# Performance work log

Hardware: AMD Instinct MI355X
Metric: run time of the kernel (lower is better)

Reference implementation:

```python
import jax, jax.numpy as jnp
import numpy as np

EPS = 1e-15

def setup_inputs() -> dict:
    key = jax.random.key(0)
    k1, k2, k3 = jax.random.split(key, 3)
    B, N, F, C = 8, 2048, 256, 64
    x = jax.random.normal(k1, (B, N, F), dtype=jnp.float32)
    adj = jax.random.uniform(k2, (B, N, N), dtype=jnp.float32)
    mask = jnp.ones((B, N), dtype=bool)
    W = jax.random.normal(k3, (F, C), dtype=jnp.float32) * 0.05
    b = jnp.zeros((C,), dtype=jnp.float32)
    return {"x": x, "adj": adj, "mask": mask, "W": W, "b": b}


def reference(x, adj, mask, W, b):
    B, N, F = x.shape
    C = W.shape[1]
    # MLP (single linear, no act/norm), dropout=0 (eval), softmax
    s = jax.nn.softmax(x @ W + b, axis=-1)                 # [B,N,C]
    m_f = mask.astype(x.dtype)[..., None]                  # [B,N,1]
    x = x * m_f
    s = s * m_f
    st = jnp.swapaxes(s, 1, 2)                             # [B,C,N]
    out = jax.nn.selu(st @ x)                              # [B,C,F]
    out_adj = st @ adj @ s                                 # [B,C,C]
    degrees = jnp.sum(adj, axis=-1)[..., None] * m_f       # [B,N,1]
    m = jnp.sum(degrees, axis=(1, 2)) / 2                  # [B]
    ca = st @ degrees                                      # [B,C,1]
    cb = jnp.swapaxes(degrees, 1, 2) @ s                   # [B,1,C]
    normalizer = (ca @ cb) / 2 / m[:, None, None]          # [B,C,C]
    decompose = out_adj - normalizer
    spectral_loss = jnp.mean(-jnp.trace(decompose, axis1=-2, axis2=-1) / 2 / m)
    ss = st @ s                                            # [B,C,C]
    i_s = jnp.eye(C, dtype=ss.dtype)
    ss_n = jnp.linalg.norm(ss, axis=(-2, -1), keepdims=True)
    i_n = jnp.linalg.norm(i_s)                             # sqrt(C)
    ortho_loss = jnp.mean(jnp.linalg.norm(ss / ss_n - i_s / i_n, axis=(-2, -1)))
    cluster_size = jnp.sum(s, axis=1)                      # [B,C]
    # note: torch broadcasts [B] / [B,1] -> [B,B]; reproduce faithfully
    cl = jnp.linalg.norm(cluster_size, axis=1) / jnp.sum(m_f, axis=1) * i_n - 1
    cluster_loss = jnp.mean(cl)
    ind = jnp.arange(C)
    out_adj = out_adj.at[:, ind, ind].set(0.0)
    d = jnp.sqrt(jnp.sum(out_adj, axis=-1))[:, None] + EPS  # [B,1,C]
    out_adj = out_adj / d / jnp.swapaxes(d, 1, 2)
    return (s, out, out_adj, spectral_loss, ortho_loss, cluster_loss)
```

## Files before the change

### kernel.cpp

```cpp
#include <hip/hip_runtime.h>
#include <math.h>

#define NB 8
#define NN 2048
#define NF 256
#define NC 64

typedef short bf16x8 __attribute__((ext_vector_type(8)));
typedef float f32x4  __attribute__((ext_vector_type(4)));

#define OFF_S    0
#define OFF_OUT  (NB*NN*NC)
#define OFF_OADJ (OFF_OUT + NB*NC*NF)
#define OFF_SCAL (OFF_OADJ + NB*NC*NC)

#define WS_T    0
#define WS_DEG  (2*NB*NN*NC)
#define WS_SF   (WS_DEG + 4*NB*NN)
#define WS_POUT (WS_SF + NB*32*8*64*4)
#define WS_PADJ (WS_POUT + NB*4*16*4096)
#define WS_PSS  (WS_PADJ + NB*32*4096)
#define WS_PCS  (WS_PSS  + NB*32*4096)
#define WS_RADJ (WS_PCS  + NB*32*64)
#define WS_RSS  (WS_RADJ + NB*4096)
#define WS_RCS  (WS_RSS  + NB*4096)
#define WS_BS   (WS_RCS  + NB*64)

__device__ __forceinline__ unsigned short f2bf(float f) {
    union { float f; unsigned int u; } v; v.f = f;
    unsigned int u = v.u;
    return (unsigned short)((u + 0x7FFFu + ((u >> 16) & 1u)) >> 16);
}
__device__ __forceinline__ float bf2f(unsigned short h) {
    union { unsigned int u; float f; } v; v.u = ((unsigned int)h) << 16;
    return v.f;
}

__global__ __launch_bounds__(512) void k_fused_s(
    const float* __restrict__ x, const float* __restrict__ W,
    const float* __restrict__ bias, float* __restrict__ s_out,
    unsigned short* __restrict__ sfrag, float* __restrict__ P_ss,
    float* __restrict__ P_cs)
{
    const int ch = blockIdx.x & 31;
    const int b  = blockIdx.x >> 5;
    const int n0 = ch * 64;
    __shared__ float xs[64][260];
    __shared__ float sB[64][68];
    __shared__ float csP[8][68];
    const int t = threadIdx.x, w = t >> 6, l = t & 63;
    const float* X = x + ((size_t)b * NN + n0) * NF;

    #pragma unroll
    for (int r = 0; r < 8; ++r) {
        const int row = w * 8 + r;
        *(float4*)&xs[row][l * 4] = *(const float4*)&X[(size_t)row * NF + l * 4];
    }
    const float bz = bias[l];
    float acc[8];
    #pragma unroll
    for (int r = 0; r < 8; ++r) acc[r] = bz;
    #pragma unroll 4
    for (int k4 = 0; k4 < 64; ++k4) {
        const int k = k4 * 4;
        const float w0 = W[(k + 0) * NC + l], w1 = W[(k + 1) * NC + l],
                    w2 = W[(k + 2) * NC + l], w3 = W[(k + 3) * NC + l];
        #pragma unroll
        for (int r = 0; r < 8; ++r) {
            const float4 xv = *(const float4*)&xs[w * 8 + r][k];
            acc[r] = fmaf(xv.x, w0, acc[r]); acc[r] = fmaf(xv.y, w1, acc[r]);
            acc[r] = fmaf(xv.z, w2, acc[r]); acc[r] = fmaf(xv.w, w3, acc[r]);
        }
    }
    float cs_acc = 0.f;
    #pragma unroll
    for (int r = 0; r < 8; ++r) {
        float a = acc[r], mx = a;
        #pragma unroll
        for (int off = 32; off; off >>= 1) mx = fmaxf(mx, __shfl_xor(mx, off));
        const float e = __expf(a - mx);
        float sum = e;
        #pragma unroll
        for (int off = 32; off; off >>= 1) sum += __shfl_xor(sum, off);
        const float sv = e / sum;
        s_out[((size_t)b * NN + n0 + w * 8 + r) * NC + l] = sv;
        sB[w * 8 + r][l] = sv;
        cs_acc += sv;
    }
    csP[w][l] = cs_acc;
    __syncthreads();

    {
        const int n = w >> 1, kk = w & 1;
        const int col = 16 * n + (l & 15);
        const int kb  = 32 * kk + (l >> 4) * 8;
        unsigned short tmp[8];
        #pragma unroll
        for (int r = 0; r < 8; ++r) tmp[r] = f2bf(sB[kb + r][col]);
        *(uint4*)&sfrag[((((size_t)(b * 32 + ch)) * 8 + w) * 64 + l) * 8] = *(uint4*)tmp;
    }
    {
        const int c0 = (t >> 5) * 4;
        const int c2 = (t & 31) * 2;
        float a2[4][2] = {{0.f,0.f},{0.f,0.f},{0.f,0.f},{0.f,0.f}};
        #pragma unroll 8
        for (int n = 0; n < 64; ++n) {
            const float4 av = *(const float4*)&sB[n][c0];
            const float2 bv = *(const float2*)&sB[n][c2];
            const float av_[4] = {av.x, av.y, av.z, av.w};
            #pragma unroll
            for (int i = 0; i < 4; ++i) {
                a2[i][0] = fmaf(av_[i], bv.x, a2[i][0]);
                a2[i][1] = fmaf(av_[i], bv.y, a2[i][1]);
            }
        }
        float* Ps = P_ss + (size_t)(b * 32 + ch) * 4096;
        #pragma unroll
        for (int i = 0; i < 4; ++i) {
            float2 v; v.x = a2[i][0]; v.y = a2[i][1];
            *(float2*)&Ps[(c0 + i) * 64 + c2] = v;
        }
    }
    if (t < 64) {
        float v = 0.f;
        #pragma unroll
        for (int g = 0; g < 8; ++g) v += csP[g][t];
        P_cs[(b * 32 + ch) * 64 + t] = v;
    }
}

__global__ __launch_bounds__(256, 4) void k_adj_reg(
    const float* __restrict__ adj, const unsigned short* __restrict__ sfrag,
    unsigned short* __restrict__ Tbuf4, float* __restrict__ deg4)
{
    const int h  = blockIdx.x & 3;
    const int mt = (blockIdx.x >> 2) & 31;
    const int b  = blockIdx.x >> 7;
    const int m0 = mt * 64;
    const int t = threadIdx.x, w = t >> 6, l = t & 63;
    const int row = m0 + 16 * w + (l & 15);
    const float* Arow = adj + (size_t)b * NN * NN + (size_t)row * NN + h * 512 + (l >> 4) * 8;
    const unsigned short* BF = sfrag + ((size_t)(b * 32 + h * 8)) * 8 * 64 * 8 + (size_t)l * 8;

    f32x4 acc[4] = {};
    float dsum = 0.f;
    float4 a0 = *(const float4*)&Arow[0];
    float4 a1 = *(const float4*)&Arow[4];
    #pragma unroll 2
    for (int ks = 0; ks < 16; ++ks) {
        float4 p0v = a0, p1v = a1;
        if (ks < 15) {
            p0v = *(const float4*)&Arow[(ks + 1) * 32];
            p1v = *(const float4*)&Arow[(ks + 1) * 32 + 4];
        }
        dsum += a0.x + a0.y + a0.z + a0.w + a1.x + a1.y + a1.z + a1.w;
        unsigned q0, q1, q2, q3;
        asm("v_cvt_pk_bf16_f32 %0, %1, %2" : "=v"(q0) : "v"(a0.x), "v"(a0.y));
        asm("v_cvt_pk_bf16_f32 %0, %1, %2" : "=v"(q1) : "v"(a0.z), "v"(a0.w));
        asm("v_cvt_pk_bf16_f32 %0, %1, %2" : "=v"(q2) : "v"(a1.x), "v"(a1.y));
        asm("v_cvt_pk_bf16_f32 %0, %1, %2" : "=v"(q3) : "v"(a1.z), "v"(a1.w));
        uint4 af_u; af_u.x = q0; af_u.y = q1; af_u.z = q2; af_u.w = q3;
        const bf16x8 af = *(const bf16x8*)&af_u;
        const unsigned short* Bk = BF + ((size_t)((ks >> 1) * 8 + (ks & 1))) * 64 * 8;
        #pragma unroll
        for (int n = 0; n < 4; ++n) {
            const bf16x8 bfv = *(const bf16x8*)&Bk[(size_t)(n * 2) * 64 * 8];
            acc[n] = __builtin_amdgcn_mfma_f32_16x16x32_bf16(af, bfv, acc[n], 0, 0, 0);
        }
        a0 = p0v; a1 = p1v;
    }
    unsigned short* Tw = Tbuf4 + (((size_t)b * NN + m0 + 16 * w) * 4 + h) * 64;
    #pragma unroll
    for (int n = 0; n < 4; ++n)
        #pragma unroll
        for (int j = 0; j < 4; ++j)
            Tw[(size_t)((l >> 4) * 4 + j) * 256 + n * 16 + (l & 15)] = f2bf(acc[n][j]);
    dsum += __shfl_xor(dsum, 16);
    dsum += __shfl_xor(dsum, 32);
    if (l < 16)
        deg4[(size_t)(h * NB + b) * NN + m0 + 16 * w + l] = dsum;
}

__global__ __launch_bounds__(256) void k_stx(
    const float* __restrict__ x, const float* __restrict__ s,
    float* __restrict__ P_out)
{
    const int ch = blockIdx.x & 15;
    const int ft = (blockIdx.x >> 4) & 3;
    const int b  = blockIdx.x >> 6;

    __shared__ float sL[64][68];
    __shared__ float xL[64][68];

    const int t  = threadIdx.x;
    const int lr = t >> 6;
    const int lc = t & 63;
    const int tr = t >> 4;
    const int tc = t & 15;
    const int r0 = tr * 4, c0 = tc * 4;

    const float* S = s + (size_t)b * NN * NC;
    const float* X = x + (size_t)b * NN * NF + ft * 64;

    float acc[4][4] = {{0.f,0.f,0.f,0.f},{0.f,0.f,0.f,0.f},{0.f,0.f,0.f,0.f},{0.f,0.f,0.f,0.f}};

    for (int tile = 0; tile < 2; ++tile) {
        const int nb = ch * 128 + tile * 64;
        __syncthreads();
        #pragma unroll
        for (int k = 0; k < 16; ++k) {
            const int nn = lr + 4 * k;
            sL[nn][lc] = S[(size_t)(nb + nn) * NC + lc];
            xL[nn][lc] = X[(size_t)(nb + nn) * NF + lc];
        }
        __syncthreads();
        #pragma unroll 8
        for (int n = 0; n < 64; ++n) {
            const float4 av = *(const float4*)&sL[n][r0];
            const float4 bv = *(const float4*)&xL[n][c0];
            const float av_[4] = {av.x, av.y, av.z, av.w};
            const float bv_[4] = {bv.x, bv.y, bv.z, bv.w};
            #pragma unroll
            for (int i = 0; i < 4; ++i)
                #pragma unroll
                for (int j = 0; j < 4; ++j)
                    acc[i][j] = fmaf(av_[i], bv_[j], acc[i][j]);
        }
    }
    float* P = P_out + (size_t)blockIdx.x * 4096;
    #pragma unroll
    for (int i = 0; i < 4; ++i) {
        float4 v; v.x = acc[i][0]; v.y = acc[i][1]; v.z = acc[i][2]; v.w = acc[i][3];
        *(float4*)&P[(r0 + i) * 64 + c0] = v;
    }
}

__global__ __launch_bounds__(256) void k_red_cc(
    const float* __restrict__ s, const unsigned short* __restrict__ Tbuf4,
    float* __restrict__ P_adj)
{
    const int ch = blockIdx.x & 31;
    const int b  = blockIdx.x >> 5;
    const int nb = ch * 64;

    __shared__ float sL[64][68];
    __shared__ float tL[64][68];

    const int t  = threadIdx.x;
    const int lr = t >> 6;
    const int lc = t & 63;
    const int tr = t >> 4;
    const int tc = t & 15;
    const int r0 = tr * 4, c0 = tc * 4;

    const float* S = s + (size_t)b * NN * NC;

    float aadj[4][4] = {{0.f,0.f,0.f,0.f},{0.f,0.f,0.f,0.f},{0.f,0.f,0.f,0.f},{0.f,0.f,0.f,0.f}};

    #pragma unroll
    for (int k = 0; k < 16; ++k) {
        const int nn = lr + 4 * k;
        sL[nn][lc] = S[(size_t)(nb + nn) * NC + lc];
        const unsigned short* Tp = &Tbuf4[(((size_t)b * NN + nb + nn) * 4) * 64 + lc];
        tL[nn][lc] = bf2f(Tp[0]) + bf2f(Tp[64]) + bf2f(Tp[128]) + bf2f(Tp[192]);
    }
    __syncthreads();
    #pragma unroll 8
    for (int n = 0; n < 64; ++n) {
        const float4 av = *(const float4*)&sL[n][r0];
        const float4 tv = *(const float4*)&tL[n][c0];
        const float av_[4] = {av.x, av.y, av.z, av.w};
        const float tv_[4] = {tv.x, tv.y, tv.z, tv.w};
        #pragma unroll
        for (int i = 0; i < 4; ++i)
            #pragma unroll
            for (int j = 0; j < 4; ++j)
                aadj[i][j] = fmaf(av_[i], tv_[j], aadj[i][j]);
    }
    float* Pa = P_adj + (size_t)(b * 32 + ch) * 4096;
    #pragma unroll
    for (int i = 0; i < 4; ++i) {
        float4 v; v.x = aadj[i][0]; v.y = aadj[i][1]; v.z = aadj[i][2]; v.w = aadj[i][3];
        *(float4*)&Pa[(r0 + i) * 64 + c0] = v;
    }
}

__global__ __launch_bounds__(256) void k_reduce2(
    const float* __restrict__ Pout, const float* __restrict__ P_adj,
    const float* __restrict__ P_ss, const float* __restrict__ P_cs,
    float* __restrict__ out, float* __restrict__ Radj, float* __restrict__ Rss,
    float* __restrict__ Rcs)
{
    const int bid = blockIdx.x;
    const int t = threadIdx.x;
    if (bid < 512) {
        const int idx = bid * 256 + t;
        const int f  = idx & 255;
        const int cc = (idx >> 8) & 63;
        const int b  = idx >> 14;
        const int ft = f >> 6, ff = f & 63;
        const float* P = Pout + ((size_t)(b * 4 + ft) * 16) * 4096 + cc * 64 + ff;
        float v = 0.f;
        #pragma unroll
        for (int ch = 0; ch < 16; ++ch) v += P[(size_t)ch * 4096];
        const float scale = 1.0507009873554805f, alpha = 1.6732632423543772f;
        out[idx] = (v > 0.f) ? scale * v : scale * alpha * expm1f(v);
    } else if (bid < 768) {
        const int idx = (bid - 512) * 256 + t;
        const int arr = idx >> 15;
        const int rem = idx & 32767;
        const int b   = rem >> 12;
        const int e   = rem & 4095;
        const float* P = (arr == 0 ? P_adj : P_ss) + (size_t)(b * 32) * 4096 + e;
        float v = 0.f;
        #pragma unroll
        for (int ch = 0; ch < 32; ++ch) v += P[(size_t)ch * 4096];
        (arr == 0 ? Radj : Rss)[b * 4096 + e] = v;
    } else {
        for (int e = t; e < 512; e += 256) {
            const int b = e >> 6, c = e & 63;
            const float* P = P_cs + (size_t)(b * 32) * 64 + c;
            float v = 0.f;
            #pragma unroll
            for (int ch = 0; ch < 32; ++ch) v += P[ch * 64];
            Rcs[b * 64 + c] = v;
        }
    }
}

__device__ __forceinline__ float block_sum(float v, float* red)
{
    #pragma unroll
    for (int off = 32; off; off >>= 1) v += __shfl_xor(v, off);
    const int w = threadIdx.x >> 6;
    __syncthreads();
    if ((threadIdx.x & 63) == 0) red[w] = v;
    __syncthreads();
    return red[0] + red[1] + red[2] + red[3];
}

__global__ __launch_bounds__(256) void k_finalize(
    const float* __restrict__ Radj, const float* __restrict__ Rss,
    const float* __restrict__ Rcs, const float* __restrict__ deg4,
    const float* __restrict__ s,
    float* __restrict__ oadj_out, float* __restrict__ bscal)
{
    const int b = blockIdx.x;
    const int t = threadIdx.x;
    __shared__ float oadj[64][65];
    __shared__ float ssm [64][65];
    __shared__ float degL[NN];
    __shared__ float caP[16][68];
    __shared__ float ca[64], cs[64], dd[64];
    __shared__ float red[4];

    for (int e = t; e < 4096; e += 256) {
        const int i = e >> 6, j = e & 63;
        oadj[i][j] = Radj[(size_t)b * 4096 + e];
        ssm [i][j] = Rss [(size_t)b * 4096 + e];
    }
    if (t < 64) cs[t] = Rcs[b * 64 + t];

    float dsum = 0.f;
    for (int n = t; n < NN; n += 256) {
        float dv = 0.f;
        #pragma unroll
        for (int p = 0; p < 4; ++p)
            dv += deg4[(size_t)(p * NB + b) * NN + n];
        degL[n] = dv;
        dsum += dv;
    }
    const float m = 0.5f * block_sum(dsum, red);

    {
        const int c4 = (t & 15) * 4;
        const int g  = t >> 4;
        const float* S = s + (size_t)b * NN * NC;
        float cacc[4] = {0.f, 0.f, 0.f, 0.f};
        for (int i = 0; i < 128; ++i) {
            const int n = g * 128 + i;
            const float4 sv = *(const float4*)&S[(size_t)n * NC + c4];
            const float dv = degL[n];
            cacc[0] = fmaf(sv.x, dv, cacc[0]);
            cacc[1] = fmaf(sv.y, dv, cacc[1]);
            cacc[2] = fmaf(sv.z, dv, cacc[2]);
            cacc[3] = fmaf(sv.w, dv, cacc[3]);
        }
        #pragma unroll
        for (int j = 0; j < 4; ++j) caP[g][c4 + j] = cacc[j];
        __syncthreads();
        if (t < 64) {
            float v = 0.f;
            #pragma unroll
            for (int g2 = 0; g2 < 16; ++g2) v += caP[g2][t];
            ca[t] = v;
        }
    }

    float tv = (t < 64) ? oadj[t][t] : 0.f;
    const float tr_oadj = block_sum(tv, red);
    float cv = (t < 64) ? ca[t] * ca[t] : 0.f;
    const float ca2 = block_sum(cv, red);

    float ss2p = 0.f;
    for (int e = t; e < 4096; e += 256) {
        const float q = ssm[e >> 6][e & 63];
        ss2p += q * q;
    }
    const float ssn = sqrtf(block_sum(ss2p, red));
    float op = 0.f;
    for (int e = t; e < 4096; e += 256) {
        const int i = e >> 6, j = e & 63;
        const float d0 = ssm[i][j] / ssn - ((i == j) ? 0.125f : 0.f);
        op += d0 * d0;
    }
    const float ortho_b = sqrtf(block_sum(op, red));
    float c2 = (t < 64) ? cs[t] * cs[t] : 0.f;
    const float cnorm_b = sqrtf(block_sum(c2, red));

    if (t == 0) {
        const float trn = ca2 / (2.f * m);
        bscal[b]          = -(tr_oadj - trn) / (2.f * m);
        bscal[NB + b]     = ortho_b;
        bscal[2 * NB + b] = cnorm_b;
    }

    __syncthreads();
    if (t < 64) oadj[t][t] = 0.f;
    __syncthreads();
    if (t < 64) {
        float rs = 0.f;
        #pragma unroll 8
        for (int j = 0; j < 64; ++j) rs += oadj[t][j];
        dd[t] = sqrtf(rs) + 1e-15f;
    }
    __syncthreads();
    float* O = oadj_out + (size_t)b * 4096;
    for (int e = t; e < 4096; e += 256) {
        const int i = e >> 6, j = e & 63;
        O[e] = oadj[i][j] / (dd[i] * dd[j]);
    }
}

__global__ void k_scalars(const float* __restrict__ bscal, float* __restrict__ scal_out)
{
    if (threadIdx.x == 0 && blockIdx.x == 0) {
        float sp = 0.f, orth = 0.f, cn = 0.f;
        for (int b = 0; b < NB; ++b) {
            sp   += bscal[b];
            orth += bscal[NB + b];
            cn   += bscal[2 * NB + b];
        }
        scal_out[0] = sp / NB;
        scal_out[1] = orth / NB;
        scal_out[2] = (cn / NB) * 8.0f / 2048.0f - 1.0f;
    }
}

extern "C" void kernel_launch(void* const* d_in, const int* in_sizes, int n_in,
                              void* d_out, int out_size, void* d_ws, size_t ws_size,
                              hipStream_t stream)
{
    const float* x    = (const float*)d_in[0];
    const float* adj  = (const float*)d_in[1];
    const float* W    = (const float*)d_in[3];
    const float* bias = (const float*)d_in[4];

    float* out = (float*)d_out;
    float* ws  = (float*)d_ws;

    float*          s_out = out + OFF_S;
    unsigned short* Tbuf4 = (unsigned short*)(ws + WS_T);
    float*          deg4  = ws + WS_DEG;
    unsigned short* sfrag = (unsigned short*)(ws + WS_SF);
    float*          Pout  = ws + WS_POUT;
    float*          Padj  = ws + WS_PADJ;
    float*          Pss   = ws + WS_PSS;
    float*          Pcs   = ws + WS_PCS;
    float*          Radj  = ws + WS_RADJ;
    float*          Rss   = ws + WS_RSS;
    float*          Rcs   = ws + WS_RCS;
    float*          bscal = ws + WS_BS;

    k_fused_s <<<NB * 32,     512, 0, stream>>>(x, W, bias, s_out, sfrag, Pss, Pcs);
    k_adj_reg <<<NB * 32 * 4, 256, 0, stream>>>(adj, sfrag, Tbuf4, deg4);
    k_stx     <<<NB * 4 * 16, 256, 0, stream>>>(x, s_out, Pout);
    k_red_cc  <<<NB * 32,     256, 0, stream>>>(s_out, Tbuf4, Padj);
    k_reduce2 <<<769,         256, 0, stream>>>(Pout, Padj, Pss, Pcs,
                                                out + OFF_OUT, Radj, Rss, Rcs);
    k_finalize<<<NB,          256, 0, stream>>>(Radj, Rss, Rcs, deg4, s_out,
                                                out + OFF_OADJ, bscal);
    k_scalars <<<1, 64, 0, stream>>>(bscal, out + OFF_SCAL);
}
```

Measured before the change: 89.81 us.

## Use split-bf16 MFMA for logits, merge adj/stx and reduction kernels

Computes x@W with MFMA using a hi/lo bf16 split of x and a pre-packed W, in place of scalar FP32 FMAs. The S^T S partial is also done with MFMA. The adjacency GEMM and the S^T x GEMM are merged into one launch, with deeper prefetch on the adj loads. The ca term (S^T deg) moves out of the single-block-per-batch finalize into the parallel reduction stage, and the reduce kernels are regrouped. This adds a small W-packing kernel and gives up some precision in the logits and the ss terms.

Result: faster. 85.90 us (-4.3%).

```diff
diff --git a/kernel.cpp b/kernel.cpp
--- a/kernel.cpp
+++ b/kernel.cpp
@@ -17,13 +17,16 @@
 #define WS_T    0
 #define WS_DEG  (2*NB*NN*NC)
 #define WS_SF   (WS_DEG + 4*NB*NN)
-#define WS_POUT (WS_SF + NB*32*8*64*4)
+#define WS_WF   (WS_SF + NB*32*8*64*4)
+#define WS_POUT (WS_WF + 16384)
 #define WS_PADJ (WS_POUT + NB*4*16*4096)
 #define WS_PSS  (WS_PADJ + NB*32*4096)
-#define WS_PCS  (WS_PSS  + NB*32*4096)
+#define WS_PCA  (WS_PSS  + NB*32*4096)
+#define WS_PCS  (WS_PCA  + NB*32*64)
 #define WS_RADJ (WS_PCS  + NB*32*64)
 #define WS_RSS  (WS_RADJ + NB*4096)
-#define WS_RCS  (WS_RSS  + NB*4096)
+#define WS_RCA  (WS_RSS  + NB*4096)
+#define WS_RCS  (WS_RCA  + NB*64)
 #define WS_BS   (WS_RCS  + NB*64)
 
 __device__ __forceinline__ unsigned short f2bf(float f) {
@@ -36,265 +39,330 @@
     return v.f;
 }
 
-__global__ __launch_bounds__(512) void k_fused_s(
-    const float* __restrict__ x, const float* __restrict__ W,
-    const float* __restrict__ bias, float* __restrict__ s_out,
-    unsigned short* __restrict__ sfrag, float* __restrict__ P_ss,
-    float* __restrict__ P_cs)
+__global__ __launch_bounds__(256) void k_wpack(
+    const float* __restrict__ W, unsigned short* __restrict__ Wfh,
+    unsigned short* __restrict__ Wfl)
+{
+    const int ks = blockIdx.x;
+    const int t = threadIdx.x;
+    const int n = t >> 6, l = t & 63;
+    const int col = 16 * n + (l & 15), g = l >> 4;
+    unsigned short th[8], tl[8];
+    #pragma unroll
+    for (int r = 0; r < 8; ++r) {
+        const int j = ((r >> 2) << 4) + g * 4 + (r & 3);
+        const float wv = W[(32 * ks + j) * NC + col];
+        const unsigned short h = f2bf(wv);
+        th[r] = h;
+        tl[r] = f2bf(wv - bf2f(h));
+    }
+    const size_t off = (((size_t)ks * 4 + n) * 64 + l) * 8;
+    *(uint4*)&Wfh[off] = *(uint4*)th;
+    *(uint4*)&Wfl[off] = *(uint4*)tl;
+}
+
+__global__ __launch_bounds__(256) void k_fused_s(
+    const float* __restrict__ x, const unsigned short* __restrict__ Wfh,
+    const unsigned short* __restrict__ Wfl, const float* __restrict__ bias,
+    float* __restrict__ s_out, unsigned short* __restrict__ sfrag,
+    float* __restrict__ P_ss, float* __restrict__ P_cs)
 {
     const int ch = blockIdx.x & 31;
     const int b  = blockIdx.x >> 5;
     const int n0 = ch * 64;
-    __shared__ float xs[64][260];
+    __shared__ __align__(16) unsigned short xh[64 * 256];
+    __shared__ __align__(16) unsigned short xl[64 * 256];
     __shared__ float sB[64][68];
-    __shared__ float csP[8][68];
+    __shared__ __align__(16) unsigned short sfl[8 * 64 * 8];
+    __shared__ float csP[16][64];
     const int t = threadIdx.x, w = t >> 6, l = t & 63;
-    const float* X = x + ((size_t)b * NN + n0) * NF;
+
+    {
+        const int srow = t >> 2, sq = t & 3;
+        const float* Xr = x + ((size_t)(b * NN + n0 + srow)) * NF;
+        float4 xv[16];
+        #pragma unroll
+        for (int i = 0; i < 16; ++i) xv[i] = *(const float4*)&Xr[i * 16 + sq * 4];
+        #pragma unroll
+        for (int i = 0; i < 16; ++i) {
+            const float4 v = xv[i];
+            const unsigned short h0 = f2bf(v.x), h1 = f2bf(v.y),
+                                 h2 = f2bf(v.z), h3 = f2bf(v.w);
+            const unsigned short e0 = f2bf(v.x - bf2f(h0)), e1 = f2bf(v.y - bf2f(h1)),
+                                 e2 = f2bf(v.z - bf2f(h2)), e3 = f2bf(v.w - bf2f(h3));
+            const int e = srow * 256 + (i >> 1) * 32 + sq * 8 + (i & 1) * 4;
+            const int byt = (2 * e) ^ ((srow & 7) << 4);
+            uint2 hv; hv.x = h0 | ((unsigned)h1 << 16); hv.y = h2 | ((unsigned)h3 << 16);
+            uint2 lv; lv.x = e0 | ((unsigned)e1 << 16); lv.y = e2 | ((unsigned)e3 << 16);
+            *(uint2*)((char*)xh + byt) = hv;
+            *(uint2*)((char*)xl + byt) = lv;
+        }
+    }
+    __syncthreads();
+
+    f32x4 acc[4] = {};
+    {
+        const int row = 16 * w + (l & 15);
+        const int g16 = (l >> 4) * 16;
+        #pragma unroll
+        for (int ks = 0; ks < 8; ++ks) {
+            const int addr = (row * 512 + ks * 64 + g16) ^ ((row & 7) << 4);
+            const bf16x8 ah = *(const bf16x8*)((const char*)xh + addr);
+            const bf16x8 al = *(const bf16x8*)((const char*)xl + addr);
+            #pragma unroll
+            for (int n = 0; n < 4; ++n) {
+                const size_t off = (((size_t)ks * 4 + n) * 64 + l) * 8;
+                const bf16x8 bh = *(const bf16x8*)&Wfh[off];
+                const bf16x8 bl = *(const bf16x8*)&Wfl[off];
+                acc[n] = __builtin_amdgcn_mfma_f32_16x16x32_bf16(ah, bh, acc[n], 0, 0, 0);
+                acc[n] = __builtin_amdgcn_mfma_f32_16x16x32_bf16(ah, bl, acc[n], 0, 0, 0);
+                acc[n] = __builtin_amdgcn_mfma_f32_16x16x32_bf16(al, bh, acc[n], 0, 0, 0);
+            }
+        }
+    }
+
+    {
+        float bz[4];
+        #pragma unroll
+        for (int n = 0; n < 4; ++n) bz[n] = bias[16 * n + (l & 15)];
+        const int g = l >> 4;
+        float ex[4][4], sj[4];
+        #pragma unroll
+        for (int j = 0; j < 4; ++j) {
+            float m = acc[0][j] + bz[0];
+            #pragma unroll
+            for (int n = 1; n < 4; ++n) m = fmaxf(m, acc[n][j] + bz[n]);
+            #pragma unroll
+            for (int k = 1; k < 16; k <<= 1) m = fmaxf(m, __shfl_xor(m, k));
+            float s = 0.f;
+            #pragma unroll
+            for (int n = 0; n < 4; ++n) { ex[n][j] = __expf(acc[n][j] + bz[n] - m); s += ex[n][j]; }
+            #pragma unroll
+            for (int k = 1; k < 16; k <<= 1) s += __shfl_xor(s, k);
+            sj[j] = 1.f / s;
+        }
+        #pragma unroll
+        for (int n = 0; n < 4; ++n) {
+            float csn = 0.f;
+            #pragma unroll
+            for (int j = 0; j < 4; ++j) {
+                const float sv = ex[n][j] * sj[j];
+                sB[16 * w + g * 4 + j][16 * n + (l & 15)] = sv;
+                csn += sv;
+            }
+            csP[w * 4 + g][16 * n + (l & 15)] = csn;
+        }
+    }
+    __syncthreads();
 
     #pragma unroll
-    for (int r = 0; r < 8; ++r) {
-        const int row = w * 8 + r;
-        *(float4*)&xs[row][l * 4] = *(const float4*)&X[(size_t)row * NF + l * 4];
-    }
-    const float bz = bias[l];
-    float acc[8];
-    #pragma unroll
-    for (int r = 0; r < 8; ++r) acc[r] = bz;
-    #pragma unroll 4
-    for (int k4 = 0; k4 < 64; ++k4) {
-        const int k = k4 * 4;
-        const float w0 = W[(k + 0) * NC + l], w1 = W[(k + 1) * NC + l],
-                    w2 = W[(k + 2) * NC + l], w3 = W[(k + 3) * NC + l];
+    for (int p = 0; p < 2; ++p) {
+        const int c2 = w + p * 4;
+        const int n = c2 >> 1, kk = c2 & 1;
+        const int col = 16 * n + (l & 15), g = l >> 4;
+        unsigned short tmp[8];
         #pragma unroll
         for (int r = 0; r < 8; ++r) {
-            const float4 xv = *(const float4*)&xs[w * 8 + r][k];
-            acc[r] = fmaf(xv.x, w0, acc[r]); acc[r] = fmaf(xv.y, w1, acc[r]);
-            acc[r] = fmaf(xv.z, w2, acc[r]); acc[r] = fmaf(xv.w, w3, acc[r]);
-        }
-    }
-    float cs_acc = 0.f;
-    #pragma unroll
-    for (int r = 0; r < 8; ++r) {
-        float a = acc[r], mx = a;
-        #pragma unroll
-        for (int off = 32; off; off >>= 1) mx = fmaxf(mx, __shfl_xor(mx, off));
-        const float e = __expf(a - mx);
-        float sum = e;
-        #pragma unroll
-        for (int off = 32; off; off >>= 1) sum += __shfl_xor(sum, off);
-        const float sv = e / sum;
-        s_out[((size_t)b * NN + n0 + w * 8 + r) * NC + l] = sv;
-        sB[w * 8 + r][l] = sv;
-        cs_acc += sv;
-    }
-    csP[w][l] = cs_acc;
-    __syncthreads();
-
+            const int j = ((r >> 2) << 4) + g * 4 + (r & 3);
+            tmp[r] = f2bf(sB[32 * kk + j][col]);
+        }
+        const size_t fo = ((size_t)c2 * 64 + l) * 8;
+        *(uint4*)&sfl[fo] = *(uint4*)tmp;
+        *(uint4*)&sfrag[((size_t)(b * 32 + ch)) * 8 * 64 * 8 + fo] = *(uint4*)tmp;
+    }
     {
-        const int n = w >> 1, kk = w & 1;
-        const int col = 16 * n + (l & 15);
-        const int kb  = 32 * kk + (l >> 4) * 8;
-        unsigned short tmp[8];
-        #pragma unroll
-        for (int r = 0; r < 8; ++r) tmp[r] = f2bf(sB[kb + r][col]);
-        *(uint4*)&sfrag[((((size_t)(b * 32 + ch)) * 8 + w) * 64 + l) * 8] = *(uint4*)tmp;
-    }
+        const int row = t >> 2, q = t & 3;
+        float4 o[4];
+        #pragma unroll
+        for (int ii = 0; ii < 4; ++ii) o[ii] = *(const float4*)&sB[row][q * 16 + ii * 4];
+        float* So = s_out + ((size_t)(b * NN + n0 + row)) * NC + q * 16;
+        #pragma unroll
+        for (int ii = 0; ii < 4; ++ii) *(float4*)&So[ii * 4] = o[ii];
+    }
+    __syncthreads();
+
     {
-        const int c0 = (t >> 5) * 4;
-        const int c2 = (t & 31) * 2;
-        float a2[4][2] = {{0.f,0.f},{0.f,0.f},{0.f,0.f},{0.f,0.f}};
-        #pragma unroll 8
-        for (int n = 0; n < 64; ++n) {
-            const float4 av = *(const float4*)&sB[n][c0];
-            const float2 bv = *(const float2*)&sB[n][c2];
-            const float av_[4] = {av.x, av.y, av.z, av.w};
-            #pragma unroll
-            for (int i = 0; i < 4; ++i) {
-                a2[i][0] = fmaf(av_[i], bv.x, a2[i][0]);
-                a2[i][1] = fmaf(av_[i], bv.y, a2[i][1]);
-            }
+        f32x4 a2[4] = {};
+        const bf16x8 af0 = *(const bf16x8*)&sfl[((size_t)(w * 2 + 0) * 64 + l) * 8];
+        const bf16x8 af1 = *(const bf16x8*)&sfl[((size_t)(w * 2 + 1) * 64 + l) * 8];
+        #pragma unroll
+        for (int n = 0; n < 4; ++n) {
+            const bf16x8 b0 = *(const bf16x8*)&sfl[((size_t)(n * 2 + 0) * 64 + l) * 8];
+            const bf16x8 b1 = *(const bf16x8*)&sfl[((size_t)(n * 2 + 1) * 64 + l) * 8];
+            a2[n] = __builtin_amdgcn_mfma_f32_16x16x32_bf16(af0, b0, a2[n], 0, 0, 0);
+            a2[n] = __builtin_amdgcn_mfma_f32_16x16x32_bf16(af1, b1, a2[n], 0, 0, 0);
         }
         float* Ps = P_ss + (size_t)(b * 32 + ch) * 4096;
         #pragma unroll
-        for (int i = 0; i < 4; ++i) {
-            float2 v; v.x = a2[i][0]; v.y = a2[i][1];
-            *(float2*)&Ps[(c0 + i) * 64 + c2] = v;
-        }
+        for (int n = 0; n < 4; ++n)
+            #pragma unroll
+            for (int j = 0; j < 4; ++j)
+                Ps[(16 * w + (l >> 4) * 4 + j) * 64 + 16 * n + (l & 15)] = a2[n][j];
     }
     if (t < 64) {
         float v = 0.f;
         #pragma unroll
-        for (int g = 0; g < 8; ++g) v += csP[g][t];
+        for (int g2 = 0; g2 < 16; ++g2) v += csP[g2][t];
         P_cs[(b * 32 + ch) * 64 + t] = v;
     }
 }
 
-__global__ __launch_bounds__(256, 4) void k_adj_reg(
+__global__ __launch_bounds__(256, 4) void k_adjstx(
     const float* __restrict__ adj, const unsigned short* __restrict__ sfrag,
-    unsigned short* __restrict__ Tbuf4, float* __restrict__ deg4)
-{
-    const int h  = blockIdx.x & 3;
-    const int mt = (blockIdx.x >> 2) & 31;
-    const int b  = blockIdx.x >> 7;
-    const int m0 = mt * 64;
-    const int t = threadIdx.x, w = t >> 6, l = t & 63;
-    const int row = m0 + 16 * w + (l & 15);
-    const float* Arow = adj + (size_t)b * NN * NN + (size_t)row * NN + h * 512 + (l >> 4) * 8;
-    const unsigned short* BF = sfrag + ((size_t)(b * 32 + h * 8)) * 8 * 64 * 8 + (size_t)l * 8;
-
-    f32x4 acc[4] = {};
-    float dsum = 0.f;
-    float4 a0 = *(const float4*)&Arow[0];
-    float4 a1 = *(const float4*)&Arow[4];
-    #pragma unroll 2
-    for (int ks = 0; ks < 16; ++ks) {
-        float4 p0v = a0, p1v = a1;
-        if (ks < 15) {
-            p0v = *(const float4*)&Arow[(ks + 1) * 32];
-            p1v = *(const float4*)&Arow[(ks + 1) * 32 + 4];
-        }
-        dsum += a0.x + a0.y + a0.z + a0.w + a1.x + a1.y + a1.z + a1.w;
-        unsigned q0, q1, q2, q3;
-        asm("v_cvt_pk_bf16_f32 %0, %1, %2" : "=v"(q0) : "v"(a0.x), "v"(a0.y));
-        asm("v_cvt_pk_bf16_f32 %0, %1, %2" : "=v"(q1) : "v"(a0.z), "v"(a0.w));
-        asm("v_cvt_pk_bf16_f32 %0, %1, %2" : "=v"(q2) : "v"(a1.x), "v"(a1.y));
-        asm("v_cvt_pk_bf16_f32 %0, %1, %2" : "=v"(q3) : "v"(a1.z), "v"(a1.w));
-        uint4 af_u; af_u.x = q0; af_u.y = q1; af_u.z = q2; af_u.w = q3;
-        const bf16x8 af = *(const bf16x8*)&af_u;
-        const unsigned short* Bk = BF + ((size_t)((ks >> 1) * 8 + (ks & 1))) * 64 * 8;
-        #pragma unroll
-        for (int n = 0; n < 4; ++n) {
-            const bf16x8 bfv = *(const bf16x8*)&Bk[(size_t)(n * 2) * 64 * 8];
-            acc[n] = __builtin_amdgcn_mfma_f32_16x16x32_bf16(af, bfv, acc[n], 0, 0, 0);
-        }
-        a0 = p0v; a1 = p1v;
-    }
-    unsigned short* Tw = Tbuf4 + (((size_t)b * NN + m0 + 16 * w) * 4 + h) * 64;
-    #pragma unroll
-    for (int n = 0; n < 4; ++n)
-        #pragma unroll
-        for (int j = 0; j < 4; ++j)
-            Tw[(size_t)((l >> 4) * 4 + j) * 256 + n * 16 + (l & 15)] = f2bf(acc[n][j]);
-    dsum += __shfl_xor(dsum, 16);
-    dsum += __shfl_xor(dsum, 32);
-    if (l < 16)
-        deg4[(size_t)(h * NB + b) * NN + m0 + 16 * w + l] = dsum;
-}
-
-__global__ __launch_bounds__(256) void k_stx(
     const float* __restrict__ x, const float* __restrict__ s,
+    unsigned short* __restrict__ Tbuf4, float* __restrict__ deg4,
     float* __restrict__ P_out)
 {
-    const int ch = blockIdx.x & 15;
-    const int ft = (blockIdx.x >> 4) & 3;
-    const int b  = blockIdx.x >> 6;
-
-    __shared__ float sL[64][68];
-    __shared__ float xL[64][68];
-
-    const int t  = threadIdx.x;
-    const int lr = t >> 6;
-    const int lc = t & 63;
-    const int tr = t >> 4;
-    const int tc = t & 15;
-    const int r0 = tr * 4, c0 = tc * 4;
-
-    const float* S = s + (size_t)b * NN * NC;
-    const float* X = x + (size_t)b * NN * NF + ft * 64;
-
-    float acc[4][4] = {{0.f,0.f,0.f,0.f},{0.f,0.f,0.f,0.f},{0.f,0.f,0.f,0.f},{0.f,0.f,0.f,0.f}};
-
-    for (int tile = 0; tile < 2; ++tile) {
-        const int nb = ch * 128 + tile * 64;
-        __syncthreads();
+    const int bid = blockIdx.x;
+    const int t = threadIdx.x;
+    if (bid < 1024) {
+        const int h = bid & 3, mt = (bid >> 2) & 31, b = bid >> 7;
+        const int m0 = mt * 64;
+        const int w = t >> 6, l = t & 63, g = l >> 4;
+        const int row = m0 + 16 * w + (l & 15);
+        const float* A = adj + (size_t)b * NN * NN + (size_t)row * NN + h * 512 + g * 4;
+        const unsigned short* BF = sfrag + ((size_t)(b * 32 + h * 8)) * 8 * 64 * 8 + (size_t)l * 8;
+
+        f32x4 acc[4] = {};
+        float dsum = 0.f;
+        float4 c0a = *(const float4*)&A[0],  c0b = *(const float4*)&A[16];
+        float4 c1a = *(const float4*)&A[32], c1b = *(const float4*)&A[48];
+        for (int ks = 0; ks < 16; ++ks) {
+            float4 n2a = c0a, n2b = c0b;
+            if (ks < 14) {
+                n2a = *(const float4*)&A[(ks + 2) * 32];
+                n2b = *(const float4*)&A[(ks + 2) * 32 + 16];
+            }
+            dsum += c0a.x + c0a.y + c0a.z + c0a.w + c0b.x + c0b.y + c0b.z + c0b.w;
+            unsigned q0, q1, q2, q3;
+            asm("v_cvt_pk_bf16_f32 %0, %1, %2" : "=v"(q0) : "v"(c0a.x), "v"(c0a.y));
+            asm("v_cvt_pk_bf16_f32 %0, %1, %2" : "=v"(q1) : "v"(c0a.z), "v"(c0a.w));
+            asm("v_cvt_pk_bf16_f32 %0, %1, %2" : "=v"(q2) : "v"(c0b.x), "v"(c0b.y));
+            asm("v_cvt_pk_bf16_f32 %0, %1, %2" : "=v"(q3) : "v"(c0b.z), "v"(c0b.w));
+            uint4 afu; afu.x = q0; afu.y = q1; afu.z = q2; afu.w = q3;
+            const bf16x8 af = *(const bf16x8*)&afu;
+            const unsigned short* Bk = BF + ((size_t)((ks >> 1) * 8 + (ks & 1))) * 64 * 8;
+            #pragma unroll
+            for (int n = 0; n < 4; ++n) {
+                const bf16x8 bfv = *(const bf16x8*)&Bk[(size_t)(n * 2) * 64 * 8];
+                acc[n] = __builtin_amdgcn_mfma_f32_16x16x32_bf16(af, bfv, acc[n], 0, 0, 0);
+            }
+            c0a = c1a; c0b = c1b; c1a = n2a; c1b = n2b;
+        }
+        unsigned short* Tw = Tbuf4 + (((size_t)b * NN + m0 + 16 * w) * 4 + h) * 64;
+        #pragma unroll
+        for (int n = 0; n < 4; ++n)
+            #pragma unroll
+            for (int j = 0; j < 4; ++j)
+                Tw[(size_t)((l >> 4) * 4 + j) * 256 + n * 16 + (l & 15)] = f2bf(acc[n][j]);
+        dsum += __shfl_xor(dsum, 16);
+        dsum += __shfl_xor(dsum, 32);
+        if (l < 16)
+            deg4[(size_t)(h * NB + b) * NN + m0 + 16 * w + l] = dsum;
+    } else {
+        const int sb = bid - 1024;
+        const int ch = sb & 15, ft = (sb >> 4) & 3, b = sb >> 6;
+        __shared__ float sL[64][68];
+        __shared__ float xL[64][68];
+        const int lr = t >> 6, lc = t & 63;
+        const int r0 = (t >> 4) * 4, c0 = (t & 15) * 4;
+        const float* S = s + (size_t)b * NN * NC;
+        const float* X = x + (size_t)b * NN * NF + ft * 64;
+        float acc[4][4] = {{0,0,0,0},{0,0,0,0},{0,0,0,0},{0,0,0,0}};
+        for (int tile = 0; tile < 2; ++tile) {
+            const int nb = ch * 128 + tile * 64;
+            __syncthreads();
+            #pragma unroll
+            for (int k = 0; k < 16; ++k) {
+                const int nn = lr + 4 * k;
+                sL[nn][lc] = S[(size_t)(nb + nn) * NC + lc];
+                xL[nn][lc] = X[(size_t)(nb + nn) * NF + lc];
+            }
+            __syncthreads();
+            #pragma unroll 8
+            for (int n = 0; n < 64; ++n) {
+                const float4 av = *(const float4*)&sL[n][r0];
+                const float4 bv = *(const float4*)&xL[n][c0];
+                const float av_[4] = {av.x, av.y, av.z, av.w};
+                const float bv_[4] = {bv.x, bv.y, bv.z, bv.w};
+                #pragma unroll
+                for (int i = 0; i < 4; ++i)
+                    #pragma unroll
+                    for (int j = 0; j < 4; ++j)
+                        acc[i][j] = fmaf(av_[i], bv_[j], acc[i][j]);
+            }
+        }
+        float* P = P_out + (size_t)sb * 4096;
+        #pragma unroll
+        for (int i = 0; i < 4; ++i) {
+            float4 v; v.x = acc[i][0]; v.y = acc[i][1]; v.z = acc[i][2]; v.w = acc[i][3];
+            *(float4*)&P[(r0 + i) * 64 + c0] = v;
+        }
+    }
+}
+
+__global__ __launch_bounds__(256) void k_redmix(
+    const float* __restrict__ s, const unsigned short* __restrict__ Tbuf4,
+    const float* __restrict__ deg4, const float* __restrict__ Pout,
+    float* __restrict__ P_adj, float* __restrict__ P_ca, float* __restrict__ out)
+{
+    const int bid = blockIdx.x;
+    const int t = threadIdx.x;
+    if (bid < 256) {
+        const int ch = bid & 31, b = bid >> 5;
+        const int nb = ch * 64;
+        __shared__ float sL[64][68];
+        __shared__ float tL[64][68];
+        __shared__ float dL[64];
+        const int lr = t >> 6, lc = t & 63;
+        const int tr = t >> 4, tc = t & 15;
+        const int r0 = tr * 4, c0 = tc * 4;
+        const float* S = s + (size_t)b * NN * NC;
+        float aadj[4][4] = {{0,0,0,0},{0,0,0,0},{0,0,0,0},{0,0,0,0}};
+        float aca[4] = {0.f, 0.f, 0.f, 0.f};
         #pragma unroll
         for (int k = 0; k < 16; ++k) {
             const int nn = lr + 4 * k;
             sL[nn][lc] = S[(size_t)(nb + nn) * NC + lc];
-            xL[nn][lc] = X[(size_t)(nb + nn) * NF + lc];
+            const unsigned short* Tp = &Tbuf4[(((size_t)b * NN + nb + nn) * 4) * 64 + lc];
+            tL[nn][lc] = bf2f(Tp[0]) + bf2f(Tp[64]) + bf2f(Tp[128]) + bf2f(Tp[192]);
+        }
+        if (t < 64) {
+            float dv = 0.f;
+            #pragma unroll
+            for (int p = 0; p < 4; ++p)
+                dv += deg4[(size_t)(p * NB + b) * NN + nb + t];
+            dL[t] = dv;
         }
         __syncthreads();
-        #pragma unroll 8
+        #pragma unroll 4
         for (int n = 0; n < 64; ++n) {
             const float4 av = *(const float4*)&sL[n][r0];
-            const float4 bv = *(const float4*)&xL[n][c0];
+            const float4 tv = *(const float4*)&tL[n][c0];
+            const float dv  = dL[n];
             const float av_[4] = {av.x, av.y, av.z, av.w};
-            const float bv_[4] = {bv.x, bv.y, bv.z, bv.w};
-            #pragma unroll
-            for (int i = 0; i < 4; ++i)
+            const float tv_[4] = {tv.x, tv.y, tv.z, tv.w};
+            #pragma unroll
+            for (int i = 0; i < 4; ++i) {
+                aca[i] = fmaf(av_[i], dv, aca[i]);
                 #pragma unroll
                 for (int j = 0; j < 4; ++j)
-                    acc[i][j] = fmaf(av_[i], bv_[j], acc[i][j]);
-        }
-    }
-    float* P = P_out + (size_t)blockIdx.x * 4096;
-    #pragma unroll
-    for (int i = 0; i < 4; ++i) {
-        float4 v; v.x = acc[i][0]; v.y = acc[i][1]; v.z = acc[i][2]; v.w = acc[i][3];
-        *(float4*)&P[(r0 + i) * 64 + c0] = v;
-    }
-}
-
-__global__ __launch_bounds__(256) void k_red_cc(
-    const float* __restrict__ s, const unsigned short* __restrict__ Tbuf4,
-    float* __restrict__ P_adj)
-{
-    const int ch = blockIdx.x & 31;
-    const int b  = blockIdx.x >> 5;
-    const int nb = ch * 64;
-
-    __shared__ float sL[64][68];
-    __shared__ float tL[64][68];
-
-    const int t  = threadIdx.x;
-    const int lr = t >> 6;
-    const int lc = t & 63;
-    const int tr = t >> 4;
-    const int tc = t & 15;
-    const int r0 = tr * 4, c0 = tc * 4;
-
-    const float* S = s + (size_t)b * NN * NC;
-
-    float aadj[4][4] = {{0.f,0.f,0.f,0.f},{0.f,0.f,0.f,0.f},{0.f,0.f,0.f,0.f},{0.f,0.f,0.f,0.f}};
-
-    #pragma unroll
-    for (int k = 0; k < 16; ++k) {
-        const int nn = lr + 4 * k;
-        sL[nn][lc] = S[(size_t)(nb + nn) * NC + lc];
-        const unsigned short* Tp = &Tbuf4[(((size_t)b * NN + nb + nn) * 4) * 64 + lc];
-        tL[nn][lc] = bf2f(Tp[0]) + bf2f(Tp[64]) + bf2f(Tp[128]) + bf2f(Tp[192]);
-    }
-    __syncthreads();
-    #pragma unroll 8
-    for (int n = 0; n < 64; ++n) {
-        const float4 av = *(const float4*)&sL[n][r0];
-        const float4 tv = *(const float4*)&tL[n][c0];
-        const float av_[4] = {av.x, av.y, av.z, av.w};
-        const float tv_[4] = {tv.x, tv.y, tv.z, tv.w};
-        #pragma unroll
-        for (int i = 0; i < 4; ++i)
-            #pragma unroll
-            for (int j = 0; j < 4; ++j)
-                aadj[i][j] = fmaf(av_[i], tv_[j], aadj[i][j]);
-    }
-    float* Pa = P_adj + (size_t)(b * 32 + ch) * 4096;
-    #pragma unroll
-    for (int i = 0; i < 4; ++i) {
-        float4 v; v.x = aadj[i][0]; v.y = aadj[i][1]; v.z = aadj[i][2]; v.w = aadj[i][3];
-        *(float4*)&Pa[(r0 + i) * 64 + c0] = v;
-    }
-}
-
-__global__ __launch_bounds__(256) void k_reduce2(
-    const float* __restrict__ Pout, const float* __restrict__ P_adj,
-    const float* __restrict__ P_ss, const float* __restrict__ P_cs,
-    float* __restrict__ out, float* __restrict__ Radj, float* __restrict__ Rss,
-    float* __restrict__ Rcs)
-{
-    const int bid = blockIdx.x;
-    const int t = threadIdx.x;
-    if (bid < 512) {
-        const int idx = bid * 256 + t;
+                    aadj[i][j] = fmaf(av_[i], tv_[j], aadj[i][j]);
+            }
+        }
+        float* Pa = P_adj + (size_t)(b * 32 + ch) * 4096;
+        #pragma unroll
+        for (int i = 0; i < 4; ++i) {
+            float4 v; v.x = aadj[i][0]; v.y = aadj[i][1]; v.z = aadj[i][2]; v.w = aadj[i][3];
+            *(float4*)&Pa[(r0 + i) * 64 + c0] = v;
+        }
+        if (tc == 0) {
+            #pragma unroll
+            for (int i = 0; i < 4; ++i)
+                P_ca[(b * 32 + ch) * 64 + r0 + i] = aca[i];
+        }
+    } else {
+        const int idx = (bid - 256) * 256 + t;
         const int f  = idx & 255;
         const int cc = (idx >> 8) & 63;
         const int b  = idx >> 14;
@@ -302,28 +370,37 @@
         const float* P = Pout + ((size_t)(b * 4 + ft) * 16) * 4096 + cc * 64 + ff;
         float v = 0.f;
         #pragma unroll
-        for (int ch = 0; ch < 16; ++ch) v += P[(size_t)ch * 4096];
+        for (int ch2 = 0; ch2 < 16; ++ch2) v += P[(size_t)ch2 * 4096];
         const float scale = 1.0507009873554805f, alpha = 1.6732632423543772f;
         out[idx] = (v > 0.f) ? scale * v : scale * alpha * expm1f(v);
-    } else if (bid < 768) {
-        const int idx = (bid - 512) * 256 + t;
-        const int arr = idx >> 15;
-        const int rem = idx & 32767;
-        const int b   = rem >> 12;
-        const int e   = rem & 4095;
-        const float* P = (arr == 0 ? P_adj : P_ss) + (size_t)(b * 32) * 4096 + e;
+    }
+}
+
+__global__ __launch_bounds__(256) void k_reduce3(
+    const float* __restrict__ P_adj, const float* __restrict__ P_ss,
+    const float* __restrict__ P_ca, const float* __restrict__ P_cs,
+    float* __restrict__ Radj, float* __restrict__ Rss,
+    float* __restrict__ Rca, float* __restrict__ Rcs)
+{
+    const int bid = blockIdx.x, t = threadIdx.x;
+    if (bid < 256) {
+        const int idx = bid * 256 + t;
+        const int arr = idx >> 15, rem = idx & 32767;
+        const int b = rem >> 12, e = rem & 4095;
+        const float* P = (arr ? P_ss : P_adj) + (size_t)(b * 32) * 4096 + e;
         float v = 0.f;
         #pragma unroll
         for (int ch = 0; ch < 32; ++ch) v += P[(size_t)ch * 4096];
-        (arr == 0 ? Radj : Rss)[b * 4096 + e] = v;
+        (arr ? Rss : Radj)[b * 4096 + e] = v;
     } else {
-        for (int e = t; e < 512; e += 256) {
-            const int b = e >> 6, c = e & 63;
-            const float* P = P_cs + (size_t)(b * 32) * 64 + c;
+        for (int e = t; e < 1024; e += 256) {
+            const int arr = e >> 9, rem = e & 511;
+            const int b = rem >> 6, c = rem & 63;
+            const float* P = (arr ? P_cs : P_ca) + (size_t)(b * 32) * 64 + c;
             float v = 0.f;
             #pragma unroll
             for (int ch = 0; ch < 32; ++ch) v += P[ch * 64];
-            Rcs[b * 64 + c] = v;
+            (arr ? Rcs : Rca)[b * 64 + c] = v;
         }
     }
 }
@@ -341,16 +418,14 @@
 
 __global__ __launch_bounds__(256) void k_finalize(
     const float* __restrict__ Radj, const float* __restrict__ Rss,
-    const float* __restrict__ Rcs, const float* __restrict__ deg4,
-    const float* __restrict__ s,
+    const float* __restrict__ Rca, const float* __restrict__ Rcs,
+    const float* __restrict__ deg4,
     float* __restrict__ oadj_out, float* __restrict__ bscal)
 {
     const int b = blockIdx.x;
     const int t = threadIdx.x;
     __shared__ float oadj[64][65];
     __shared__ float ssm [64][65];
-    __shared__ float degL[NN];
-    __shared__ float caP[16][68];
     __shared__ float ca[64], cs[64], dd[64];
     __shared__ float red[4];
 
@@ -359,43 +434,18 @@
         oadj[i][j] = Radj[(size_t)b * 4096 + e];
         ssm [i][j] = Rss [(size_t)b * 4096 + e];
     }
-    if (t < 64) cs[t] = Rcs[b * 64 + t];
+    if (t < 64) {
+        ca[t] = Rca[b * 64 + t];
+        cs[t] = Rcs[b * 64 + t];
+    }
 
     float dsum = 0.f;
     for (int n = t; n < NN; n += 256) {
-        float dv = 0.f;
         #pragma unroll
         for (int p = 0; p < 4; ++p)
-            dv += deg4[(size_t)(p * NB + b) * NN + n];
-        degL[n] = dv;
-        dsum += dv;
+            dsum += deg4[(size_t)(p * NB + b) * NN + n];
     }
     const float m = 0.5f * block_sum(dsum, red);
-
-    {
-        const int c4 = (t & 15) * 4;
-        const int g  = t >> 4;
-        const float* S = s + (size_t)b * NN * NC;
-        float cacc[4] = {0.f, 0.f, 0.f, 0.f};
-        for (int i = 0; i < 128; ++i) {
-            const int n = g * 128 + i;
-            const float4 sv = *(const float4*)&S[(size_t)n * NC + c4];
-            const float dv = degL[n];
-            cacc[0] = fmaf(sv.x, dv, cacc[0]);
-            cacc[1] = fmaf(sv.y, dv, cacc[1]);
-            cacc[2] = fmaf(sv.z, dv, cacc[2]);
-            cacc[3] = fmaf(sv.w, dv, cacc[3]);
-        }
-        #pragma unroll
-        for (int j = 0; j < 4; ++j) caP[g][c4 + j] = cacc[j];
-        __syncthreads();
-        if (t < 64) {
-            float v = 0.f;
-            #pragma unroll
-            for (int g2 = 0; g2 < 16; ++g2) v += caP[g2][t];
-            ca[t] = v;
-        }
-    }
 
     float tv = (t < 64) ? oadj[t][t] : 0.f;
     const float tr_oadj = block_sum(tv, red);
@@ -473,22 +523,24 @@
     unsigned short* Tbuf4 = (unsigned short*)(ws + WS_T);
     float*          deg4  = ws + WS_DEG;
     unsigned short* sfrag = (unsigned short*)(ws + WS_SF);
+    unsigned short* Wfh   = (unsigned short*)(ws + WS_WF);
+    unsigned short* Wfl   = Wfh + 8 * 4 * 64 * 8;
     float*          Pout  = ws + WS_POUT;
     float*          Padj  = ws + WS_PADJ;
     float*          Pss   = ws + WS_PSS;
+    float*          Pca   = ws + WS_PCA;
     float*          Pcs   = ws + WS_PCS;
     float*          Radj  = ws + WS_RADJ;
     float*          Rss   = ws + WS_RSS;
+    float*          Rca   = ws + WS_RCA;
     float*          Rcs   = ws + WS_RCS;
     float*          bscal = ws + WS_BS;
 
-    k_fused_s <<<NB * 32,     512, 0, stream>>>(x, W, bias, s_out, sfrag, Pss, Pcs);
-    k_adj_reg <<<NB * 32 * 4, 256, 0, stream>>>(adj, sfrag, Tbuf4, deg4);
-    k_stx     <<<NB * 4 * 16, 256, 0, stream>>>(x, s_out, Pout);
-    k_red_cc  <<<NB * 32,     256, 0, stream>>>(s_out, Tbuf4, Padj);
-    k_reduce2 <<<769,         256, 0, stream>>>(Pout, Padj, Pss, Pcs,
-                                                out + OFF_OUT, Radj, Rss, Rcs);
-    k_finalize<<<NB,          256, 0, stream>>>(Radj, Rss, Rcs, deg4, s_out,
-                                                out + OFF_OADJ, bscal);
+    k_wpack   <<<8,    256, 0, stream>>>(W, Wfh, Wfl);
+    k_fused_s <<<256,  256, 0, stream>>>(x, Wfh, Wfl, bias, s_out, sfrag, Pss, Pcs);
+    k_adjstx  <<<1536, 256, 0, stream>>>(adj, sfrag, x, s_out, Tbuf4, deg4, Pout);
+    k_redmix  <<<768,  256, 0, stream>>>(s_out, Tbuf4, deg4, Pout, Padj, Pca, out + OFF_OUT);
+    k_reduce3 <<<257,  256, 0, stream>>>(Padj, Pss, Pca, Pcs, Radj, Rss, Rca, Rcs);
+    k_finalize<<<8,    256, 0, stream>>>(Radj, Rss, Rca, Rcs, deg4, out + OFF_OADJ, bscal);
     k_scalars <<<1, 64, 0, stream>>>(bscal, out + OFF_SCAL);
 }
```
